# Kernel optimization log

Measured on AMD Instinct MI355X. Metric: run time of the kernel, lower is better.

Reference implementation:

```python
import jax, jax.numpy as jnp
import numpy as np

SCALE_RES = 16
EPS_NORM = 1e-12  # torch F.normalize default eps


def _l2_normalize(x, axis):
    n = jnp.sqrt(jnp.sum(x * x, axis=axis, keepdims=True))
    return x / jnp.maximum(n, EPS_NORM)


def setup_inputs() -> dict:
    key = jax.random.key(0)
    k1, k2, k3, k4 = jax.random.split(key, 4)
    N, K, H, W, M = 16, 17, 256, 256, 30
    L = K * H * W // SCALE_RES  # 69632 flattened tag locations
    tags = jax.random.normal(k1, (N, K, H, W), dtype=jnp.float32)
    loc = jax.random.randint(k2, (N, M, K, 1), 0, L)
    vis = jax.random.randint(k3, (N, M, K, 1), 0, 2)  # visibility flag
    joints = jnp.concatenate([loc, vis], axis=-1).astype(jnp.int64)
    box_scales = jax.random.uniform(k4, (N, M), dtype=jnp.float32)
    scale_dist = jnp.arange(0.5 / SCALE_RES, 1.0, 1.0 / SCALE_RES, dtype=jnp.float32)
    return {"tags": tags, "joints": joints, "box_scales": box_scales, "scale_dist": scale_dist}


def _ae_loss(tags, box_scales, scale_dist, loc, vis):
    # tags: [N,K,H,W]; loc: [N,M,K] int; vis: [N,M,K] bool; box_scales: [N,M]
    N = tags.shape[0]
    S = scale_dist.shape[0]
    M, K = vis.shape[1], vis.shape[2]
    tags_flat = tags.reshape(N, -1, S)  # [N, L, S]
    gathered = jnp.take_along_axis(tags_flat, loc.reshape(N, M * K, 1), axis=1)
    gathered = gathered.reshape(N, M, K, S)  # [N,M,K,S]

    visf = vis.astype(tags.dtype)           # [N,M,K]
    cnt = visf.sum(-1)                      # [N,M] visible joints per person
    valid = cnt > 0
    safe_cnt = jnp.maximum(cnt, 1.0)
    mean_tag = (gathered * visf[..., None]).sum(2) / safe_cnt[..., None]  # [N,M,S]

    # pull: mean over (visible joints x S) of squared deviation from person mean
    pull_p = ((gathered - mean_tag[:, :, None, :]) ** 2 * visf[..., None]).sum((2, 3)) / (safe_cnt * S)

    # scale embedding target and cosine to normalized |mean tag|
    gap = jnp.abs(box_scales[..., None] - scale_dist)      # [N,M,S]
    tgt = _l2_normalize(1.0 / (gap + 1e-10), -1)
    pred = _l2_normalize(jnp.abs(mean_tag), -1)
    d_scale_p = 1.0 - (tgt * pred).sum(-1)                 # [N,M]

    validf = valid.astype(tags.dtype)
    n = validf.sum(-1)                                      # [N] num people w/ tags
    safe_n = jnp.maximum(n, 1.0)
    pull_img = (pull_p * validf).sum(-1) / safe_n           # 0 when n==0; /1 when n==1 (== unchanged)
    scale_img = (d_scale_p * validf).sum(-1) / safe_n

    # push: mean over off-diagonal valid pairs of exp(-||ta-tb||^2), scaled by 0.5
    diff = ((mean_tag[:, :, None, :] - mean_tag[:, None, :, :]) ** 2).sum(-1)  # [N,M,M]
    pair = validf[:, :, None] * validf[:, None, :] * (1.0 - jnp.eye(M, dtype=tags.dtype))
    push_sum = (jnp.exp(-diff) * pair).sum((1, 2))
    push_img = jnp.where(n >= 2.0, 0.5 * push_sum / jnp.maximum(n * (n - 1.0), 1.0), 0.0)

    return pull_img.mean(), push_img.mean(), scale_img.mean()


def reference(tags, joints, box_scales, scale_dist):
    loc = joints[..., 0]
    vis = joints[..., 1] > 0
    return _ae_loss(tags, box_scales, scale_dist, loc, vis)
```

## Files before the change

kernel.cpp:

```cpp
#include <hip/hip_runtime.h>

#define N_IMG 16
#define M_PPL 30
#define K_JNT 17
#define S_DIM 16
#define HW (256 * 256)
#define IMG_STRIDE (K_JNT * HW)

__global__ __launch_bounds__(512) void ae_per_image(
    const float* __restrict__ tags,
    const int* __restrict__ joints,
    const float* __restrict__ box_scales,
    const float* __restrict__ scale_dist,
    float* __restrict__ ws)
{
    const int n = blockIdx.x;
    const int t = threadIdx.x;

    __shared__ float g_sh[M_PPL][K_JNT][S_DIM];
    __shared__ float mean_sh[M_PPL][S_DIM];
    __shared__ int   loc_sh[M_PPL][K_JNT];
    __shared__ float vis_sh[M_PPL][K_JNT];
    __shared__ float cnt_sh[M_PPL];
    __shared__ float pull_sh[M_PPL];
    __shared__ float dsc_sh[M_PPL];
    __shared__ float sd_sh[S_DIM];
    __shared__ float red_sh[8];

    if (t < S_DIM) sd_sh[t] = scale_dist[t];
    if (t < M_PPL * K_JNT) {
        int m = t / K_JNT, k = t % K_JNT;
        const int* jp = joints + (((long)n * M_PPL + m) * K_JNT + k) * 2;
        loc_sh[m][k] = jp[0];
        vis_sh[m][k] = (jp[1] > 0) ? 1.0f : 0.0f;
    }
    __syncthreads();

    const int m = t >> 4;
    const int s = t & 15;
    float meanv = 0.0f;
    float cnt = 0.0f;
    if (m < M_PPL) {
        const float* tbase = tags + (size_t)n * IMG_STRIDE + s;
        float sum = 0.0f;
        #pragma unroll
        for (int k = 0; k < K_JNT; ++k) {
            float v = vis_sh[m][k];
            float g = tbase[(size_t)loc_sh[m][k] * S_DIM];
            g_sh[m][k][s] = g;
            sum += v * g;
            cnt += v;
        }
        meanv = sum / fmaxf(cnt, 1.0f);
        mean_sh[m][s] = meanv;
        if (s == 0) cnt_sh[m] = cnt;
    }
    __syncthreads();

    if (m < M_PPL) {
        float p = 0.0f;
        #pragma unroll
        for (int k = 0; k < K_JNT; ++k) {
            float d = g_sh[m][k][s] - meanv;
            p += vis_sh[m][k] * d * d;
        }
        float bs  = box_scales[n * M_PPL + m];
        float tgt = 1.0f / (fabsf(bs - sd_sh[s]) + 1e-10f);
        float am  = fabsf(meanv);
        float pr2 = am * am;
        float tg2 = tgt * tgt;
        float dt  = am * tgt;
        #pragma unroll
        for (int o = 1; o < 16; o <<= 1) {
            p   += __shfl_xor(p, o);
            pr2 += __shfl_xor(pr2, o);
            tg2 += __shfl_xor(tg2, o);
            dt  += __shfl_xor(dt, o);
        }
        if (s == 0) {
            pull_sh[m] = p / (fmaxf(cnt, 1.0f) * (float)S_DIM);
            float normP = fmaxf(sqrtf(pr2), 1e-12f);
            float normT = fmaxf(sqrtf(tg2), 1e-12f);
            dsc_sh[m] = 1.0f - dt / (normP * normT);
        }
    }
    __syncthreads();

    float psum = 0.0f;
    for (int p = t; p < M_PPL * M_PPL; p += 512) {
        int a = p / M_PPL, b = p - a * M_PPL;
        if (a != b && cnt_sh[a] > 0.0f && cnt_sh[b] > 0.0f) {
            float d2 = 0.0f;
            #pragma unroll
            for (int ss = 0; ss < S_DIM; ++ss) {
                float d = mean_sh[a][ss] - mean_sh[b][ss];
                d2 += d * d;
            }
            psum += expf(-d2);
        }
    }
    #pragma unroll
    for (int o = 1; o < 64; o <<= 1) psum += __shfl_xor(psum, o);
    if ((t & 63) == 0) red_sh[t >> 6] = psum;
    __syncthreads();

    if (t == 0) {
        float push_total = 0.0f;
        #pragma unroll
        for (int w = 0; w < 8; ++w) push_total += red_sh[w];
        float nval = 0.0f, pullsum = 0.0f, scsum = 0.0f;
        for (int mm = 0; mm < M_PPL; ++mm) {
            if (cnt_sh[mm] > 0.0f) {
                nval += 1.0f;
                pullsum += pull_sh[mm];
                scsum   += dsc_sh[mm];
            }
        }
        float safe_n = fmaxf(nval, 1.0f);
        float push_img = (nval >= 2.0f)
                           ? 0.5f * push_total / fmaxf(nval * (nval - 1.0f), 1.0f)
                           : 0.0f;
        ws[n * 3 + 0] = pullsum / safe_n;
        ws[n * 3 + 1] = push_img;
        ws[n * 3 + 2] = scsum / safe_n;
    }
}

__global__ void ae_finalize(const float* __restrict__ ws, float* __restrict__ out)
{
    int t = threadIdx.x;
    if (t < 3) {
        float sacc = 0.0f;
        #pragma unroll
        for (int n = 0; n < N_IMG; ++n) sacc += ws[n * 3 + t];
        out[t] = sacc / (float)N_IMG;
    }
}

extern "C" void kernel_launch(void* const* d_in, const int* in_sizes, int n_in,
                              void* d_out, int out_size, void* d_ws, size_t ws_size,
                              hipStream_t stream) {
    const float* tags       = (const float*)d_in[0];
    const int*   joints     = (const int*)d_in[1];
    const float* box_scales = (const float*)d_in[2];
    const float* scale_dist = (const float*)d_in[3];
    float* out = (float*)d_out;
    float* ws  = (float*)d_ws;

    ae_per_image<<<N_IMG, 512, 0, stream>>>(tags, joints, box_scales, scale_dist, ws);
    ae_finalize<<<1, 64, 0, stream>>>(ws, out);
}
```

Measured before the change: 11.61 us.

## Fuse finalize into per-image kernel with atomics and single-pass pull variance

Drops the separate finalize kernel; each block now atomically adds its scaled per-image losses into the output, which is zeroed by a memset. Joint locations are loaded as int2 and spread across lanes with shuffles instead of being staged in shared memory. The pull term is computed in one pass from sum and sum of squares, so the gathered-tags buffer and a barrier go away. The push loop only visits a<b pairs and uses fast exp, and the per-person reductions use a warp shuffle instead of a serial loop. In exchange it adds a memset launch, float atomics with nondeterministic summation order, and possible cancellation error in the single-pass variance.

```diff
diff --git a/kernel.cpp b/kernel.cpp
--- a/kernel.cpp
+++ b/kernel.cpp
@@ -7,69 +7,57 @@
 #define HW (256 * 256)
 #define IMG_STRIDE (K_JNT * HW)
 
-__global__ __launch_bounds__(512) void ae_per_image(
+__global__ __launch_bounds__(512) void ae_fused(
     const float* __restrict__ tags,
     const int* __restrict__ joints,
     const float* __restrict__ box_scales,
     const float* __restrict__ scale_dist,
-    float* __restrict__ ws)
+    float* __restrict__ out)
 {
     const int n = blockIdx.x;
     const int t = threadIdx.x;
+    const int m = t >> 4;
+    const int s = t & 15;
 
-    __shared__ float g_sh[M_PPL][K_JNT][S_DIM];
     __shared__ float mean_sh[M_PPL][S_DIM];
-    __shared__ int   loc_sh[M_PPL][K_JNT];
-    __shared__ float vis_sh[M_PPL][K_JNT];
     __shared__ float cnt_sh[M_PPL];
     __shared__ float pull_sh[M_PPL];
     __shared__ float dsc_sh[M_PPL];
-    __shared__ float sd_sh[S_DIM];
     __shared__ float red_sh[8];
 
-    if (t < S_DIM) sd_sh[t] = scale_dist[t];
-    if (t < M_PPL * K_JNT) {
-        int m = t / K_JNT, k = t % K_JNT;
-        const int* jp = joints + (((long)n * M_PPL + m) * K_JNT + k) * 2;
-        loc_sh[m][k] = jp[0];
-        vis_sh[m][k] = (jp[1] > 0) ? 1.0f : 0.0f;
-    }
-    __syncthreads();
+    if (m < M_PPL) {
+        const int* jb = joints + ((n * M_PPL + m) * K_JNT) * 2;
+        const int2 js  = ((const int2*)jb)[s];
+        const int2 j16 = ((const int2*)jb)[16];
+        const float sd = scale_dist[s];
+        const float bs = box_scales[n * M_PPL + m];
+        const float* tbase = tags + (size_t)n * IMG_STRIDE + s;
 
-    const int m = t >> 4;
-    const int s = t & 15;
-    float meanv = 0.0f;
-    float cnt = 0.0f;
-    if (m < M_PPL) {
-        const float* tbase = tags + (size_t)n * IMG_STRIDE + s;
-        float sum = 0.0f;
+        float sum = 0.f, sum2 = 0.f, cnt = 0.f;
         #pragma unroll
-        for (int k = 0; k < K_JNT; ++k) {
-            float v = vis_sh[m][k];
-            float g = tbase[(size_t)loc_sh[m][k] * S_DIM];
-            g_sh[m][k][s] = g;
-            sum += v * g;
-            cnt += v;
+        for (int k = 0; k < 16; ++k) {
+            int loc = __shfl(js.x, k, 16);
+            int vis = __shfl(js.y, k, 16);
+            float g = tbase[(size_t)loc * S_DIM];
+            float v = (vis > 0) ? 1.f : 0.f;
+            sum  += v * g;
+            sum2 += v * g * g;
+            cnt  += v;
         }
-        meanv = sum / fmaxf(cnt, 1.0f);
-        mean_sh[m][s] = meanv;
-        if (s == 0) cnt_sh[m] = cnt;
-    }
-    __syncthreads();
+        {
+            float g = tbase[(size_t)j16.x * S_DIM];
+            float v = (j16.y > 0) ? 1.f : 0.f;
+            sum += v * g; sum2 += v * g * g; cnt += v;
+        }
 
-    if (m < M_PPL) {
-        float p = 0.0f;
-        #pragma unroll
-        for (int k = 0; k < K_JNT; ++k) {
-            float d = g_sh[m][k][s] - meanv;
-            p += vis_sh[m][k] * d * d;
-        }
-        float bs  = box_scales[n * M_PPL + m];
-        float tgt = 1.0f / (fabsf(bs - sd_sh[s]) + 1e-10f);
-        float am  = fabsf(meanv);
-        float pr2 = am * am;
-        float tg2 = tgt * tgt;
-        float dt  = am * tgt;
+        const float safe_cnt = fmaxf(cnt, 1.f);
+        const float mean = sum / safe_cnt;
+        mean_sh[m][s] = mean;
+
+        float p   = sum2 - cnt * mean * mean;
+        float am  = fabsf(mean);
+        float tgt = 1.f / (fabsf(bs - sd) + 1e-10f);
+        float pr2 = am * am, tg2 = tgt * tgt, dt = am * tgt;
         #pragma unroll
         for (int o = 1; o < 16; o <<= 1) {
             p   += __shfl_xor(p, o);
@@ -78,62 +66,59 @@
             dt  += __shfl_xor(dt, o);
         }
         if (s == 0) {
-            pull_sh[m] = p / (fmaxf(cnt, 1.0f) * (float)S_DIM);
+            cnt_sh[m]  = cnt;
+            pull_sh[m] = p / (safe_cnt * (float)S_DIM);
             float normP = fmaxf(sqrtf(pr2), 1e-12f);
             float normT = fmaxf(sqrtf(tg2), 1e-12f);
-            dsc_sh[m] = 1.0f - dt / (normP * normT);
+            dsc_sh[m]  = 1.f - dt / (normP * normT);
         }
     }
     __syncthreads();
 
-    float psum = 0.0f;
-    for (int p = t; p < M_PPL * M_PPL; p += 512) {
-        int a = p / M_PPL, b = p - a * M_PPL;
-        if (a != b && cnt_sh[a] > 0.0f && cnt_sh[b] > 0.0f) {
-            float d2 = 0.0f;
+    float psum = 0.f;
+    for (int pidx = t; pidx < M_PPL * M_PPL; pidx += 512) {
+        int a = pidx / M_PPL, b = pidx - a * M_PPL;
+        if (a < b && cnt_sh[a] > 0.f && cnt_sh[b] > 0.f) {
+            float d2 = 0.f;
             #pragma unroll
             for (int ss = 0; ss < S_DIM; ++ss) {
                 float d = mean_sh[a][ss] - mean_sh[b][ss];
                 d2 += d * d;
             }
-            psum += expf(-d2);
+            psum += __expf(-d2);
         }
     }
     #pragma unroll
     for (int o = 1; o < 64; o <<= 1) psum += __shfl_xor(psum, o);
     if ((t & 63) == 0) red_sh[t >> 6] = psum;
+
+    float pullsum = 0.f, scsum = 0.f, nval = 0.f;
+    if (t < 32) {
+        bool v = (t < M_PPL) && (cnt_sh[t] > 0.f);
+        pullsum = v ? pull_sh[t] : 0.f;
+        scsum   = v ? dsc_sh[t]  : 0.f;
+        nval    = v ? 1.f        : 0.f;
+        #pragma unroll
+        for (int o = 1; o < 32; o <<= 1) {
+            pullsum += __shfl_xor(pullsum, o, 32);
+            scsum   += __shfl_xor(scsum, o, 32);
+            nval    += __shfl_xor(nval, o, 32);
+        }
+    }
     __syncthreads();
 
     if (t == 0) {
-        float push_total = 0.0f;
+        float push_total = 0.f;
         #pragma unroll
         for (int w = 0; w < 8; ++w) push_total += red_sh[w];
-        float nval = 0.0f, pullsum = 0.0f, scsum = 0.0f;
-        for (int mm = 0; mm < M_PPL; ++mm) {
-            if (cnt_sh[mm] > 0.0f) {
-                nval += 1.0f;
-                pullsum += pull_sh[mm];
-                scsum   += dsc_sh[mm];
-            }
-        }
-        float safe_n = fmaxf(nval, 1.0f);
-        float push_img = (nval >= 2.0f)
-                           ? 0.5f * push_total / fmaxf(nval * (nval - 1.0f), 1.0f)
-                           : 0.0f;
-        ws[n * 3 + 0] = pullsum / safe_n;
-        ws[n * 3 + 1] = push_img;
-        ws[n * 3 + 2] = scsum / safe_n;
-    }
-}
-
-__global__ void ae_finalize(const float* __restrict__ ws, float* __restrict__ out)
-{
-    int t = threadIdx.x;
-    if (t < 3) {
-        float sacc = 0.0f;
-        #pragma unroll
-        for (int n = 0; n < N_IMG; ++n) sacc += ws[n * 3 + t];
-        out[t] = sacc / (float)N_IMG;
+        float safe_n = fmaxf(nval, 1.f);
+        float push_img = (nval >= 2.f)
+                           ? push_total / fmaxf(nval * (nval - 1.f), 1.f)
+                           : 0.f;
+        const float inv_n = 1.f / (float)N_IMG;
+        atomicAdd(&out[0], pullsum / safe_n * inv_n);
+        atomicAdd(&out[1], push_img * inv_n);
+        atomicAdd(&out[2], scsum / safe_n * inv_n);
     }
 }
 
@@ -145,8 +130,7 @@
     const float* box_scales = (const float*)d_in[2];
     const float* scale_dist = (const float*)d_in[3];
     float* out = (float*)d_out;
-    float* ws  = (float*)d_ws;
 
-    ae_per_image<<<N_IMG, 512, 0, stream>>>(tags, joints, box_scales, scale_dist, ws);
-    ae_finalize<<<1, 64, 0, stream>>>(ws, out);
+    hipMemsetAsync(out, 0, 3 * sizeof(float), stream);
+    ae_fused<<<N_IMG, 512, 0, stream>>>(tags, joints, box_scales, scale_dist, out);
 }
```

New measurement: 14.11 us. +21.5%, slower.
